# Optimization experiments

Hardware: AMD Instinct MI355X
Metric: run time of the kernel (lower is better)

The kernel has to match this reference:

```python
import jax, jax.numpy as jnp
import numpy as np

DIM = 1024
HEADS = 16
DIM_HEAD = 64
WINDOW = 256  # sliding window size == block size
NEG = -1e9


def rms_norm(x, gamma, size):
    # F.normalize(x, dim=-1) * sqrt(size) * gamma
    nrm = jnp.sqrt(jnp.sum(x * x, axis=-1, keepdims=True))
    return x / jnp.maximum(nrm, 1e-12) * (size ** 0.5) * gamma


def sliding_window_attention(q, k, v, window):
    # q,k,v: [b, h, S, d]; causal local attention: key j valid iff i-window <= j <= i
    b, h, S, d = q.shape
    Bk = window
    nb = S // Bk
    qb = q.reshape(b, h, nb, Bk, d)
    kb = k.reshape(b, h, nb, Bk, d)
    vb = v.reshape(b, h, nb, Bk, d)
    # previous key/value block (zeros for block 0; masked out below)
    k_prev = jnp.pad(kb, ((0, 0), (0, 0), (1, 0), (0, 0), (0, 0)))[:, :, :nb]
    v_prev = jnp.pad(vb, ((0, 0), (0, 0), (1, 0), (0, 0), (0, 0)))[:, :, :nb]
    kctx = jnp.concatenate([k_prev, kb], axis=3)  # [b,h,nb,2Bk,d]
    vctx = jnp.concatenate([v_prev, vb], axis=3)
    scale = 1.0 / jnp.sqrt(jnp.asarray(d, q.dtype))
    scores = jnp.einsum('bhnqd,bhnkd->bhnqk', qb, kctx) * scale  # [b,h,nb,Bk,2Bk]
    qi = jnp.arange(Bk)[:, None]          # local query index
    kj = jnp.arange(2 * Bk)[None, :]      # local key index (offset -Bk rel to block start)
    diff = Bk + qi - kj                   # global i - j
    base = (diff >= 0) & (diff <= window)  # [Bk, 2Bk]
    blk = jnp.arange(nb)[:, None, None]
    key_exists = ((blk - 1) * Bk + kj[None]) >= 0  # [nb,1,2Bk] -> broadcast
    mask = base[None] & key_exists                 # [nb,Bk,2Bk]
    scores = jnp.where(mask[None, None], scores, NEG)
    attn = jax.nn.softmax(scores, axis=-1)
    out = jnp.einsum('bhnqk,bhnkd->bhnqd', attn, vctx)
    return out.reshape(b, h, S, d)


def setup_inputs() -> dict:
    key = jax.random.key(0)
    ks = jax.random.split(key, 6)
    b, S = 2, 4096
    dim_inner = HEADS * DIM_HEAD
    x = jax.random.normal(ks[0], (b, S, DIM), dtype=jnp.float32)
    gamma = jnp.ones((DIM,), dtype=jnp.float32)
    W_qkv = jax.random.normal(ks[1], (DIM, 3 * dim_inner), dtype=jnp.float32) * 0.02
    W_gates = jax.random.normal(ks[2], (DIM, HEADS), dtype=jnp.float32) * 0.02
    b_gates = jnp.zeros((HEADS,), dtype=jnp.float32)
    W_out = jax.random.normal(ks[3], (dim_inner, DIM), dtype=jnp.float32) * 0.02
    return {"x": x, "gamma": gamma, "W_qkv": W_qkv, "W_gates": W_gates,
            "b_gates": b_gates, "W_out": W_out}


def reference(x, gamma, W_qkv, W_gates, b_gates, W_out):
    b, S, dim = x.shape
    xn = rms_norm(x, gamma, dim)
    qkv = xn @ W_qkv                                    # [b,S,3*h*d]
    qkv = qkv.reshape(b, S, 3, HEADS, DIM_HEAD)
    q, k, v = [jnp.transpose(t, (0, 2, 1, 3)) for t in
               (qkv[:, :, 0], qkv[:, :, 1], qkv[:, :, 2])]  # [b,h,S,d]
    out = sliding_window_attention(q, k, v, WINDOW)      # [b,h,S,d]
    gates = xn @ W_gates + b_gates                       # [b,S,h]
    out = out * jax.nn.sigmoid(jnp.transpose(gates, (0, 2, 1)))[..., None]
    out = jnp.transpose(out, (0, 2, 1, 3)).reshape(b, S, HEADS * DIM_HEAD)
    return out @ W_out
```

## Files before the change

### kernel.cpp

```cpp
#include <hip/hip_runtime.h>
#include <hip/hip_bf16.h>
#include <stdint.h>

typedef __bf16 bf16;
typedef __bf16 bf16x4 __attribute__((ext_vector_type(4)));
typedef __bf16 bf16x8 __attribute__((ext_vector_type(8)));
typedef float f32x4 __attribute__((ext_vector_type(4)));

#define GLOBAL_AS __attribute__((address_space(1)))
#define LDS_AS __attribute__((address_space(3)))

__device__ __forceinline__ void g2lds16(const bf16* g, bf16* l) {
  __builtin_amdgcn_global_load_lds((const GLOBAL_AS void*)g, (LDS_AS void*)l, 16, 0, 0);
}

__global__ __launch_bounds__(256) void rmsnorm_kernel(
    const float* __restrict__ x, const float* __restrict__ gamma,
    bf16* __restrict__ xn) {
  __shared__ float wss[4];
  const int t = threadIdx.x;
  const size_t row = blockIdx.x;
  const float* xr = x + row * 1024;

  float4 xv = *(const float4*)&xr[t * 4];
  float v[4] = {xv.x, xv.y, xv.z, xv.w};
  float ss = v[0]*v[0] + v[1]*v[1] + v[2]*v[2] + v[3]*v[3];
#pragma unroll
  for (int mm = 1; mm < 64; mm <<= 1) ss += __shfl_xor(ss, mm);
  if ((t & 63) == 0) wss[t >> 6] = ss;
  __syncthreads();
  ss = wss[0] + wss[1] + wss[2] + wss[3];
  float inv = 32.0f / sqrtf(fmaxf(ss, 1e-24f));

  float4 gv = *(const float4*)&gamma[t * 4];
  float gvv[4] = {gv.x, gv.y, gv.z, gv.w};
  bf16x4 outv;
#pragma unroll
  for (int i = 0; i < 4; ++i) outv[i] = (bf16)(v[i] * inv * gvv[i]);
  *(bf16x4*)&xn[row * 1024 + t * 4] = outv;
}

__global__ void transpose_f32_bf16(const float* __restrict__ in, bf16* __restrict__ out,
                                   int R, int C) {
  __shared__ bf16 tile[32][33];
  const int tx = threadIdx.x, ty = threadIdx.y;
  const int c0 = blockIdx.x * 32, r0 = blockIdx.y * 32;
#pragma unroll
  for (int i = 0; i < 32; i += 8)
    tile[ty + i][tx] = (bf16)in[(size_t)(r0 + ty + i) * C + c0 + tx];
  __syncthreads();
#pragma unroll
  for (int i = 0; i < 32; i += 8)
    out[(size_t)(c0 + ty + i) * R + r0 + tx] = tile[tx][ty + i];
}

__global__ __launch_bounds__(256) void wg_transpose(const float* __restrict__ Wg,
                                                    bf16* __restrict__ BtAug) {
  int idx = blockIdx.x * 256 + threadIdx.x;
  int n = idx >> 10, k = idx & 1023;
  BtAug[(size_t)(3072 + n) * 1024 + k] = (bf16)Wg[(size_t)k * 16 + n];
}

template <typename OutT>
__global__ __launch_bounds__(256) void gemm_bt_128(
    const bf16* __restrict__ A, const bf16* __restrict__ Bt,
    OutT* __restrict__ C, int M, int N, int K) {
  __shared__ bf16 lA[128 * 64];
  __shared__ bf16 lB[128 * 64];
  const int t = threadIdx.x;
  const int w = t >> 6, lane = t & 63;
  const int col0 = lane & 15, quad = lane >> 4;
  const int m0 = blockIdx.y * 128, n0 = blockIdx.x * 128;
  const int wr = (w >> 1) * 64, wc = (w & 1) * 64;

  const int lrow = t >> 3;
  const int sswz = (((t & 7) ^ (lrow & 7)) << 3);

  f32x4 acc[4][4] = {};

  for (int k0 = 0; k0 < K; k0 += 64) {
    __syncthreads();
#pragma unroll
    for (int c = 0; c < 4; ++c) {
      g2lds16(A  + (size_t)(m0 + c * 32 + lrow) * K + k0 + sswz, &lA[c * 2048 + w * 512]);
      g2lds16(Bt + (size_t)(n0 + c * 32 + lrow) * K + k0 + sswz, &lB[c * 2048 + w * 512]);
    }
    __syncthreads();

#pragma unroll
    for (int kh = 0; kh < 2; ++kh) {
      bf16x8 af[4], bfr[4];
#pragma unroll
      for (int i = 0; i < 4; ++i) {
        int row = wr + i * 16 + col0;
        af[i] = *(const bf16x8*)&lA[row * 64 + (((kh * 4 + quad) ^ (row & 7)) << 3)];
      }
#pragma unroll
      for (int j = 0; j < 4; ++j) {
        int row = wc + j * 16 + col0;
        bfr[j] = *(const bf16x8*)&lB[row * 64 + (((kh * 4 + quad) ^ (row & 7)) << 3)];
      }
#pragma unroll
      for (int i = 0; i < 4; ++i)
#pragma unroll
        for (int j = 0; j < 4; ++j)
          acc[i][j] = __builtin_amdgcn_mfma_f32_16x16x32_bf16(af[i], bfr[j], acc[i][j], 0, 0, 0);
    }
  }

#pragma unroll
  for (int i = 0; i < 4; ++i)
#pragma unroll
    for (int j = 0; j < 4; ++j)
#pragma unroll
      for (int r = 0; r < 4; ++r) {
        int row = m0 + wr + i * 16 + quad * 4 + r;
        int col = n0 + wc + j * 16 + col0;
        C[(size_t)row * N + col] = (OutT)acc[i][j][r];
      }
}

template <typename OutT>
__global__ __launch_bounds__(512, 2) void gemm_bt_256(
    const bf16* __restrict__ A, const bf16* __restrict__ Bt,
    OutT* __restrict__ C, int M, int N, int K) {
  extern __shared__ bf16 lds[];
  bf16* A0 = lds;
  bf16* B0 = lds + 16384;
  bf16* A1 = lds + 32768;
  bf16* B1 = lds + 49152;

  const int t = threadIdx.x;
  const int w = t >> 6, lane = t & 63;
  const int wm = w >> 2, wn = w & 3;
  const int col0 = lane & 15, quad = lane >> 4;
  const int sswz = (((t & 7) ^ ((t >> 3) & 7)) << 3);

  int nwg = gridDim.x * gridDim.y;
  int bid = blockIdx.y * gridDim.x + blockIdx.x;
  int swz = bid;
  if ((nwg & 7) == 0) swz = (bid & 7) * (nwg >> 3) + (bid >> 3);
  const int n0 = (swz % gridDim.x) * 256;
  const int m0 = (swz / gridDim.x) * 256;

  const bf16* Abase = A + (size_t)m0 * (size_t)K;

  auto stageA = [&](int ks, int c, bf16* dstA) {
    int row = c * 64 + (t >> 3);
    g2lds16(Abase + (size_t)row * K + ks + sswz, dstA + c * 4096 + w * 512);
  };
  auto stageB = [&](int ks, int c, bf16* dstB) {
    int gr = n0 + c * 64 + (t >> 3);
    gr = (gr < N) ? gr : (N - 1);
    g2lds16(Bt + (size_t)gr * (size_t)K + ks + sswz, dstB + c * 4096 + w * 512);
  };

  f32x4 acc[4][2][4] = {};
  const int NT = K >> 6;

  stageB(0, 0, B0); stageB(0, 1, B0); stageB(0, 2, B0); stageB(0, 3, B0);
  stageA(0, 0, A0);
  stageA(0, 1, A0); stageA(0, 2, A0); stageA(0, 3, A0);
  asm volatile("s_waitcnt vmcnt(3)" ::: "memory");
  __builtin_amdgcn_s_barrier();

  for (int T = 0; T < NT; ++T) {
    bf16* cA = (T & 1) ? A1 : A0;
    bf16* cB = (T & 1) ? B1 : B0;
    bf16* nA = (T & 1) ? A0 : A1;
    bf16* nB = (T & 1) ? B0 : B1;
    int tn = T + 1;
    int kn = ((tn < NT) ? tn : 0) << 6;

    bf16x8 bv[4][2];
#pragma unroll
    for (int q = 0; q < 4; ++q) {
      if (q == 0) {
#pragma unroll
        for (int nj = 0; nj < 4; ++nj) {
          int br = wn * 64 + nj * 16 + col0;
#pragma unroll
          for (int ks = 0; ks < 2; ++ks)
            bv[nj][ks] = *(const bf16x8*)&cB[br * 64 + (((ks * 4 + quad) ^ (br & 7)) << 3)];
        }
      }
      bf16x8 af[2][2];
#pragma unroll
      for (int m2 = 0; m2 < 2; ++m2) {
        int ar = q * 64 + wm * 32 + m2 * 16 + col0;
#pragma unroll
        for (int ks = 0; ks < 2; ++ks)
          af[m2][ks] = *(const bf16x8*)&cA[ar * 64 + (((ks * 4 + quad) ^ (ar & 7)) << 3)];
      }
      if (q == 0)      { stageA(kn, 0, nA); stageB(kn, 0, nB); }
      else if (q == 1) { stageB(kn, 1, nB); stageB(kn, 2, nB); }
      else if (q == 2) { stageB(kn, 3, nB); stageA(kn, 1, nA); }
      else             { stageA(kn, 2, nA); stageA(kn, 3, nA); }
      if (q == 0)      asm volatile("s_waitcnt vmcnt(4)" ::: "memory");
      else if (q == 1) asm volatile("s_waitcnt vmcnt(5)" ::: "memory");
      else if (q == 2) asm volatile("s_waitcnt vmcnt(6)" ::: "memory");
      else             asm volatile("s_waitcnt vmcnt(3)" ::: "memory");
      __builtin_amdgcn_s_barrier();
      asm volatile("s_waitcnt lgkmcnt(0)" ::: "memory");
      __builtin_amdgcn_sched_barrier(0);
      __builtin_amdgcn_s_setprio(1);
#pragma unroll
      for (int ks = 0; ks < 2; ++ks)
#pragma unroll
        for (int m2 = 0; m2 < 2; ++m2)
#pragma unroll
          for (int nj = 0; nj < 4; ++nj)
            acc[q][m2][nj] = __builtin_amdgcn_mfma_f32_16x16x32_bf16(
                af[m2][ks], bv[nj][ks], acc[q][m2][nj], 0, 0, 0);
      __builtin_amdgcn_s_setprio(0);
      __builtin_amdgcn_s_barrier();
    }
  }
  asm volatile("s_waitcnt vmcnt(0)" ::: "memory");

#pragma unroll
  for (int q = 0; q < 4; ++q)
#pragma unroll
    for (int m2 = 0; m2 < 2; ++m2)
#pragma unroll
      for (int nj = 0; nj < 4; ++nj) {
        int col = n0 + wn * 64 + nj * 16 + col0;
        if (col < N) {
          size_t base = (size_t)(m0 + q * 64 + wm * 32 + m2 * 16 + quad * 4) * N + col;
#pragma unroll
          for (int r = 0; r < 4; ++r)
            C[base + (size_t)r * N] = (OutT)acc[q][m2][nj][r];
        }
      }
}

#define NEG_BIG -1e30f
__global__ __launch_bounds__(256) void attn_kernel(
    const bf16* __restrict__ qkv, const float* __restrict__ bg,
    bf16* __restrict__ attnO) {
  __shared__ bf16 lQ[64 * 64];
  __shared__ bf16 lKV[320 * 64];
  __shared__ bf16 lP[4 * 16 * 32];

  const int t = threadIdx.x;
  const int w = t >> 6, lane = t & 63;
  const int col0 = lane & 15, quad = lane >> 4;

  const int blk = blockIdx.x;
  const int g = blk & 63;
  const int h = (blk >> 6) & 15;
  const int bb = blk >> 10;
  const int qs = g * 64;

  const size_t rs = 3200;
  const bf16* qbase = qkv + ((size_t)bb * 4096) * rs + h * 64;

  for (int c = t; c < 64 * 8; c += 256) {
    int row = c >> 3, ck = c & 7;
    *(uint4*)&lQ[row * 64 + ((ck ^ (row & 7)) << 3)] =
        *(const uint4*)(qbase + (size_t)(qs + row) * rs + ck * 8);
  }
  for (int c = t; c < 320 * 8; c += 256) {
    int row = c >> 3, ck = c & 7;
    int j = qs - 256 + row;
    uint4 val = {0, 0, 0, 0};
    if (j >= 0) val = *(const uint4*)(qbase + 1024 + (size_t)j * rs + ck * 8);
    *(uint4*)&lKV[row * 64 + ((ck ^ (row & 7)) << 3)] = val;
  }
  __syncthreads();

  const int qrow = w * 16 + col0;
  bf16x8 a0 = *(const bf16x8*)&lQ[qrow * 64 + ((quad ^ (qrow & 7)) << 3)];
  bf16x8 a1 = *(const bf16x8*)&lQ[qrow * 64 + (((4 + quad) ^ (qrow & 7)) << 3)];
  f32x4 s[20];
#pragma unroll
  for (int kt = 0; kt < 20; ++kt) {
    int krow = kt * 16 + col0;
    bf16x8 b0 = *(const bf16x8*)&lKV[krow * 64 + ((quad ^ (krow & 7)) << 3)];
    bf16x8 b1 = *(const bf16x8*)&lKV[krow * 64 + (((4 + quad) ^ (krow & 7)) << 3)];
    f32x4 z = {};
    z = __builtin_amdgcn_mfma_f32_16x16x32_bf16(a0, b0, z, 0, 0, 0);
    z = __builtin_amdgcn_mfma_f32_16x16x32_bf16(a1, b1, z, 0, 0, 0);
    s[kt] = z;
  }
  __syncthreads();

  {
    const int jl = t & 31, dg = t >> 5;
#pragma unroll
    for (int cc = 0; cc < 10; ++cc) {
      int j = qs - 256 + cc * 32 + jl;
      bf16 tmp[8];
      if (j >= 0) {
        *(uint4*)tmp = *(const uint4*)(qbase + 2048 + (size_t)j * rs + dg * 8);
      } else {
#pragma unroll
        for (int d2 = 0; d2 < 8; ++d2) tmp[d2] = (bf16)0.f;
      }
      int ck = cc * 4 + (jl >> 3);
      int wi = jl & 7;
#pragma unroll
      for (int d2 = 0; d2 < 8; ++d2) {
        int d = dg * 8 + d2;
        lKV[d * 320 + ((ck ^ (d & 7)) << 3) + wi] = tmp[d2];
      }
    }
  }

  float mrow[4] = {NEG_BIG, NEG_BIG, NEG_BIG, NEG_BIG};
  float lrow[4] = {0, 0, 0, 0};
#pragma unroll
  for (int kt = 0; kt < 20; ++kt) {
    int c = kt * 16 + col0;
#pragma unroll
    for (int r = 0; r < 4; ++r) {
      int ql = w * 16 + quad * 4 + r;
      bool valid = (c >= ql) && (c <= ql + 256) && (qs - 256 + c >= 0);
      float sv = valid ? s[kt][r] * 0.125f : NEG_BIG;
      s[kt][r] = sv;
      mrow[r] = fmaxf(mrow[r], sv);
    }
  }
#pragma unroll
  for (int mm = 1; mm < 16; mm <<= 1)
#pragma unroll
    for (int r = 0; r < 4; ++r) mrow[r] = fmaxf(mrow[r], __shfl_xor(mrow[r], mm));
#pragma unroll
  for (int kt = 0; kt < 20; ++kt)
#pragma unroll
    for (int r = 0; r < 4; ++r) {
      float p = __expf(s[kt][r] - mrow[r]);
      s[kt][r] = p;
      lrow[r] += p;
    }
#pragma unroll
  for (int mm = 1; mm < 16; mm <<= 1)
#pragma unroll
    for (int r = 0; r < 4; ++r) lrow[r] += __shfl_xor(lrow[r], mm);

  __syncthreads();

  f32x4 o[4] = {};
  bf16* pw = &lP[w * 512];
#pragma unroll
  for (int kc = 0; kc < 10; ++kc) {
#pragma unroll
    for (int r = 0; r < 4; ++r) {
      pw[(quad * 4 + r) * 32 + col0]      = (bf16)s[2 * kc][r];
      pw[(quad * 4 + r) * 32 + 16 + col0] = (bf16)s[2 * kc + 1][r];
    }
    asm volatile("s_waitcnt lgkmcnt(0)" ::: "memory");
    bf16x8 pa = *(const bf16x8*)&pw[col0 * 32 + quad * 8];
#pragma unroll
    for (int n = 0; n < 4; ++n) {
      int d = n * 16 + col0;
      bf16x8 bvv = *(const bf16x8*)&lKV[d * 320 + (((kc * 4 + quad) ^ (d & 7)) << 3)];
      o[n] = __builtin_amdgcn_mfma_f32_16x16x32_bf16(pa, bvv, o[n], 0, 0, 0);
    }
  }

  const bf16* gbase = qkv + ((size_t)bb * 4096) * rs + 3072 + h;
  const float bgh = bg[h];
#pragma unroll
  for (int r = 0; r < 4; ++r) {
    int ql = w * 16 + quad * 4 + r;
    int srow = qs + ql;
    float logit = (float)gbase[(size_t)srow * rs] + bgh;
    float gate = 1.f / (1.f + __expf(-logit));
    float scale = gate / lrow[r];
#pragma unroll
    for (int n = 0; n < 4; ++n)
      attnO[((size_t)bb * 4096 + srow) * 1024 + h * 64 + n * 16 + col0] =
          (bf16)(o[n][r] * scale);
  }
}

extern "C" void kernel_launch(void* const* d_in, const int* in_sizes, int n_in,
                              void* d_out, int out_size, void* d_ws, size_t ws_size,
                              hipStream_t stream) {
  const float *x = nullptr, *gamma = nullptr, *Wqkv = nullptr,
              *Wg = nullptr, *bg = nullptr, *Wout = nullptr;
  for (int i = 0; i < n_in; ++i) {
    switch (in_sizes[i]) {
      case 8388608: x     = (const float*)d_in[i]; break;
      case 1024:    gamma = (const float*)d_in[i]; break;
      case 3145728: Wqkv  = (const float*)d_in[i]; break;
      case 16384:   Wg    = (const float*)d_in[i]; break;
      case 16:      bg    = (const float*)d_in[i]; break;
      case 1048576: Wout  = (const float*)d_in[i]; break;
    }
  }
  float* out = (float*)d_out;

  static bool attr_done = false;
  if (!attr_done) {
    hipFuncSetAttribute(reinterpret_cast<const void*>(&gemm_bt_256<bf16>),
                        hipFuncAttributeMaxDynamicSharedMemorySize, 131072);
    attr_done = true;
  }

  char* ws = (char*)d_ws;
  bf16* qkv   = (bf16*)ws;  ws += (size_t)8192 * 3200 * 2;
  bf16* xn    = (bf16*)ws;
  bf16* attnO = (bf16*)ws;  ws += (size_t)8192 * 1024 * 2;
  bf16* BtAug = (bf16*)ws;  ws += (size_t)3200 * 1024 * 2;
  bf16* WoutT = (bf16*)ws;  ws += (size_t)1024 * 1024 * 2;

  hipMemsetAsync(BtAug + (size_t)3088 * 1024, 0, (size_t)112 * 1024 * 2, stream);

  rmsnorm_kernel<<<8192, 256, 0, stream>>>(x, gamma, xn);
  transpose_f32_bf16<<<dim3(3072 / 32, 1024 / 32), dim3(32, 8), 0, stream>>>(Wqkv, BtAug, 1024, 3072);
  wg_transpose<<<64, 256, 0, stream>>>(Wg, BtAug);
  transpose_f32_bf16<<<dim3(1024 / 32, 1024 / 32), dim3(32, 8), 0, stream>>>(Wout, WoutT, 1024, 1024);
  gemm_bt_256<bf16><<<dim3(13, 32), 512, 131072, stream>>>(xn, BtAug, qkv, 8192, 3200, 1024);
  attn_kernel<<<2048, 256, 0, stream>>>(qkv, bg, attnO);
  gemm_bt_128<float><<<dim3(1024 / 128, 8192 / 128), 256, 0, stream>>>(attnO, WoutT, out, 8192, 1024, 1024);
}
```

Baseline: 257.5 us.

## Restructure attention kernel: transposed MFMA, async K load, shuffle-based P exchange

Rewrites the sliding-window attention kernel so each lane owns one query row: Q is loaded straight into registers, and the MFMA operands are swapped so scores come out transposed. Softmax reductions then need only two cross-lane shuffles. K tiles are loaded into LDS with global_load_lds, and P is repacked through register shuffles instead of an LDS scratch buffer. The kernel also sets an occupancy hint, remaps block indices so blocks interleave across batch and head, and writes output as vectors. The aim is to cut LDS traffic, reduction shuffles and barriers, at the cost of more complex lane remapping and hand-placed waitcnt and barrier instructions.

```diff
diff --git a/kernel.cpp b/kernel.cpp
--- a/kernel.cpp
+++ b/kernel.cpp
@@ -235,18 +235,18 @@
 }
 
 #define NEG_BIG -1e30f
-__global__ __launch_bounds__(256) void attn_kernel(
+__global__ __launch_bounds__(256, 4) void attn_kernel(
     const bf16* __restrict__ qkv, const float* __restrict__ bg,
     bf16* __restrict__ attnO) {
-  __shared__ bf16 lQ[64 * 64];
   __shared__ bf16 lKV[320 * 64];
-  __shared__ bf16 lP[4 * 16 * 32];
 
   const int t = threadIdx.x;
-  const int w = t >> 6, lane = t & 63;
+  const int lane = t & 63;
+  const int w = t >> 6;
   const int col0 = lane & 15, quad = lane >> 4;
 
-  const int blk = blockIdx.x;
+  const int bid = blockIdx.x;
+  const int blk = ((bid & 7) << 8) | (bid >> 3);
   const int g = blk & 63;
   const int h = (blk >> 6) & 15;
   const int bb = blk >> 10;
@@ -255,123 +255,119 @@
   const size_t rs = 3200;
   const bf16* qbase = qkv + ((size_t)bb * 4096) * rs + h * 64;
 
-  for (int c = t; c < 64 * 8; c += 256) {
-    int row = c >> 3, ck = c & 7;
-    *(uint4*)&lQ[row * 64 + ((ck ^ (row & 7)) << 3)] =
-        *(const uint4*)(qbase + (size_t)(qs + row) * rs + ck * 8);
-  }
-  for (int c = t; c < 320 * 8; c += 256) {
-    int row = c >> 3, ck = c & 7;
-    int j = qs - 256 + row;
-    uint4 val = {0, 0, 0, 0};
-    if (j >= 0) val = *(const uint4*)(qbase + 1024 + (size_t)j * rs + ck * 8);
-    *(uint4*)&lKV[row * 64 + ((ck ^ (row & 7)) << 3)] = val;
-  }
-  __syncthreads();
-
-  const int qrow = w * 16 + col0;
-  bf16x8 a0 = *(const bf16x8*)&lQ[qrow * 64 + ((quad ^ (qrow & 7)) << 3)];
-  bf16x8 a1 = *(const bf16x8*)&lQ[qrow * 64 + (((4 + quad) ^ (qrow & 7)) << 3)];
-  f32x4 s[20];
+  {
+    const int lr = t >> 3;
+    const int sswz = ((t & 7) ^ (lr & 7)) << 3;
+#pragma unroll
+    for (int c = 0; c < 10; ++c) {
+      int j = qs - 256 + c * 32 + lr;
+      j = (j < 0) ? 0 : j;
+      g2lds16(qbase + 1024 + (size_t)j * rs + sswz, &lKV[c * 2048 + w * 512]);
+    }
+  }
+  __builtin_amdgcn_sched_barrier(0);
+  const int ql = w * 16 + col0;
+  const int srow = qs + ql;
+  const bf16x8 bq0 = *(const bf16x8*)(qbase + (size_t)srow * rs + quad * 8);
+  const bf16x8 bq1 = *(const bf16x8*)(qbase + (size_t)srow * rs + 32 + quad * 8);
+  const float logit = (float)qkv[((size_t)bb * 4096 + srow) * rs + 3072 + h];
+  asm volatile("s_waitcnt vmcnt(3)" ::: "memory");
+  asm volatile("s_barrier" ::: "memory");
+
+  f32x4 z[20];
 #pragma unroll
   for (int kt = 0; kt < 20; ++kt) {
-    int krow = kt * 16 + col0;
-    bf16x8 b0 = *(const bf16x8*)&lKV[krow * 64 + ((quad ^ (krow & 7)) << 3)];
-    bf16x8 b1 = *(const bf16x8*)&lKV[krow * 64 + (((4 + quad) ^ (krow & 7)) << 3)];
-    f32x4 z = {};
-    z = __builtin_amdgcn_mfma_f32_16x16x32_bf16(a0, b0, z, 0, 0, 0);
-    z = __builtin_amdgcn_mfma_f32_16x16x32_bf16(a1, b1, z, 0, 0, 0);
-    s[kt] = z;
-  }
-  __syncthreads();
+    const int kr = kt * 16 + col0;
+    bf16x8 a0 = *(const bf16x8*)&lKV[kr * 64 + ((quad ^ (kr & 7)) << 3)];
+    bf16x8 a1 = *(const bf16x8*)&lKV[kr * 64 + (((4 + quad) ^ (kr & 7)) << 3)];
+    f32x4 zz = {};
+    zz = __builtin_amdgcn_mfma_f32_16x16x32_bf16(a0, bq0, zz, 0, 0, 0);
+    zz = __builtin_amdgcn_mfma_f32_16x16x32_bf16(a1, bq1, zz, 0, 0, 0);
+    z[kt] = zz;
+  }
+  asm volatile("s_barrier" ::: "memory");
 
   {
     const int jl = t & 31, dg = t >> 5;
 #pragma unroll
     for (int cc = 0; cc < 10; ++cc) {
       int j = qs - 256 + cc * 32 + jl;
+      j = (j < 0) ? 0 : j;
       bf16 tmp[8];
-      if (j >= 0) {
-        *(uint4*)tmp = *(const uint4*)(qbase + 2048 + (size_t)j * rs + dg * 8);
-      } else {
-#pragma unroll
-        for (int d2 = 0; d2 < 8; ++d2) tmp[d2] = (bf16)0.f;
-      }
-      int ck = cc * 4 + (jl >> 3);
-      int wi = jl & 7;
+      *(uint4*)tmp = *(const uint4*)(qbase + 2048 + (size_t)j * rs + dg * 8);
+      const int ck = cc * 4 + (jl >> 3);
+      const int wi = jl & 7;
 #pragma unroll
       for (int d2 = 0; d2 < 8; ++d2) {
-        int d = dg * 8 + d2;
+        const int d = dg * 8 + d2;
         lKV[d * 320 + ((ck ^ (d & 7)) << 3) + wi] = tmp[d2];
       }
     }
   }
 
-  float mrow[4] = {NEG_BIG, NEG_BIG, NEG_BIG, NEG_BIG};
-  float lrow[4] = {0, 0, 0, 0};
-#pragma unroll
-  for (int kt = 0; kt < 20; ++kt) {
-    int c = kt * 16 + col0;
+  float m = NEG_BIG;
+#pragma unroll
+  for (int kt = 0; kt < 20; ++kt)
 #pragma unroll
     for (int r = 0; r < 4; ++r) {
-      int ql = w * 16 + quad * 4 + r;
-      bool valid = (c >= ql) && (c <= ql + 256) && (qs - 256 + c >= 0);
-      float sv = valid ? s[kt][r] * 0.125f : NEG_BIG;
-      s[kt][r] = sv;
-      mrow[r] = fmaxf(mrow[r], sv);
-    }
-  }
-#pragma unroll
-  for (int mm = 1; mm < 16; mm <<= 1)
-#pragma unroll
-    for (int r = 0; r < 4; ++r) mrow[r] = fmaxf(mrow[r], __shfl_xor(mrow[r], mm));
+      const int c = kt * 16 + quad * 4 + r;
+      const bool valid = (c >= ql) && (c <= ql + 256) && (qs - 256 + c >= 0);
+      const float sv = valid ? z[kt][r] * 0.125f : NEG_BIG;
+      z[kt][r] = sv;
+      m = fmaxf(m, sv);
+    }
+  m = fmaxf(m, __shfl_xor(m, 16));
+  m = fmaxf(m, __shfl_xor(m, 32));
+  float l = 0.f;
 #pragma unroll
   for (int kt = 0; kt < 20; ++kt)
 #pragma unroll
     for (int r = 0; r < 4; ++r) {
-      float p = __expf(s[kt][r] - mrow[r]);
-      s[kt][r] = p;
-      lrow[r] += p;
-    }
-#pragma unroll
-  for (int mm = 1; mm < 16; mm <<= 1)
-#pragma unroll
-    for (int r = 0; r < 4; ++r) lrow[r] += __shfl_xor(lrow[r], mm);
+      const float p = __expf(z[kt][r] - m);
+      z[kt][r] = p;
+      l += p;
+    }
+  l += __shfl_xor(l, 16);
+  l += __shfl_xor(l, 32);
 
   __syncthreads();
 
   f32x4 o[4] = {};
-  bf16* pw = &lP[w * 512];
+  const int sl0 = col0 + ((quad & 1) << 5);
+  const bool hi = quad >= 2;
 #pragma unroll
   for (int kc = 0; kc < 10; ++kc) {
-#pragma unroll
-    for (int r = 0; r < 4; ++r) {
-      pw[(quad * 4 + r) * 32 + col0]      = (bf16)s[2 * kc][r];
-      pw[(quad * 4 + r) * 32 + 16 + col0] = (bf16)s[2 * kc + 1][r];
-    }
-    asm volatile("s_waitcnt lgkmcnt(0)" ::: "memory");
-    bf16x8 pa = *(const bf16x8*)&pw[col0 * 32 + quad * 8];
+    uint32_t Pl0, Pl1, Ph0, Ph1;
+    asm("v_cvt_pk_bf16_f32 %0, %1, %2" : "=v"(Pl0) : "v"(z[2*kc][0]),   "v"(z[2*kc][1]));
+    asm("v_cvt_pk_bf16_f32 %0, %1, %2" : "=v"(Pl1) : "v"(z[2*kc][2]),   "v"(z[2*kc][3]));
+    asm("v_cvt_pk_bf16_f32 %0, %1, %2" : "=v"(Ph0) : "v"(z[2*kc+1][0]), "v"(z[2*kc+1][1]));
+    asm("v_cvt_pk_bf16_f32 %0, %1, %2" : "=v"(Ph1) : "v"(z[2*kc+1][2]), "v"(z[2*kc+1][3]));
+    uint32_t w0l = __shfl((int)Pl0, sl0),      w0h = __shfl((int)Ph0, sl0);
+    uint32_t w1l = __shfl((int)Pl1, sl0),      w1h = __shfl((int)Ph1, sl0);
+    uint32_t w2l = __shfl((int)Pl0, sl0 + 16), w2h = __shfl((int)Ph0, sl0 + 16);
+    uint32_t w3l = __shfl((int)Pl1, sl0 + 16), w3h = __shfl((int)Ph1, sl0 + 16);
+    union { uint32_t u[4]; bf16x8 v; } pu;
+    pu.u[0] = hi ? w0h : w0l;
+    pu.u[1] = hi ? w1h : w1l;
+    pu.u[2] = hi ? w2h : w2l;
+    pu.u[3] = hi ? w3h : w3l;
 #pragma unroll
     for (int n = 0; n < 4; ++n) {
-      int d = n * 16 + col0;
-      bf16x8 bvv = *(const bf16x8*)&lKV[d * 320 + (((kc * 4 + quad) ^ (d & 7)) << 3)];
-      o[n] = __builtin_amdgcn_mfma_f32_16x16x32_bf16(pa, bvv, o[n], 0, 0, 0);
-    }
-  }
-
-  const bf16* gbase = qkv + ((size_t)bb * 4096) * rs + 3072 + h;
-  const float bgh = bg[h];
-#pragma unroll
-  for (int r = 0; r < 4; ++r) {
-    int ql = w * 16 + quad * 4 + r;
-    int srow = qs + ql;
-    float logit = (float)gbase[(size_t)srow * rs] + bgh;
-    float gate = 1.f / (1.f + __expf(-logit));
-    float scale = gate / lrow[r];
-#pragma unroll
-    for (int n = 0; n < 4; ++n)
-      attnO[((size_t)bb * 4096 + srow) * 1024 + h * 64 + n * 16 + col0] =
-          (bf16)(o[n][r] * scale);
+      const int d = n * 16 + col0;
+      bf16x8 av = *(const bf16x8*)&lKV[d * 320 + (((kc * 4 + quad) ^ (d & 7)) << 3)];
+      o[n] = __builtin_amdgcn_mfma_f32_16x16x32_bf16(av, pu.v, o[n], 0, 0, 0);
+    }
+  }
+
+  const float gate = 1.f / (1.f + __expf(-(logit + bg[h])));
+  const float scale = gate / l;
+  bf16* obase = attnO + ((size_t)bb * 4096 + srow) * 1024 + h * 64;
+#pragma unroll
+  for (int n = 0; n < 4; ++n) {
+    bf16x4 ov;
+#pragma unroll
+    for (int r = 0; r < 4; ++r) ov[r] = (bf16)(o[n][r] * scale);
+    *(bf16x4*)&obase[n * 16 + quad * 4] = ov;
   }
 }
 
```

After: 235.1 us. 1.1x faster.
